# Performance work log

Measured on AMD Instinct MI355X. Metric: run time of the kernel, lower is better.

## Reference

```python
import jax, jax.numpy as jnp
import numpy as np

B, T, D_IN, H, NC = 256, 512, 40, 128, 7


def _lstm_dir(x, W_ih, W_hh, b):
    # x: [B,T,D]; W_ih: [4H,D]; W_hh: [4H,H]; b: [4H] (b_ih+b_hh combined)
    pre = jnp.einsum('btd,gd->btg', x, W_ih) + b  # [B,T,4H]
    h0 = jnp.zeros((x.shape[0], W_hh.shape[1]), x.dtype)
    c0 = jnp.zeros_like(h0)

    def step(carry, p_t):
        h, c = carry
        g = p_t + h @ W_hh.T  # [B,4H]
        i, f, gg, o = jnp.split(g, 4, axis=-1)  # PyTorch gate order: i,f,g,o
        i = jax.nn.sigmoid(i)
        f = jax.nn.sigmoid(f)
        gg = jnp.tanh(gg)
        o = jax.nn.sigmoid(o)
        c = f * c + i * gg
        h = o * jnp.tanh(c)
        return (h, c), h

    _, hs = jax.lax.scan(step, (h0, c0), jnp.swapaxes(pre, 0, 1))  # [T,B,H]
    return jnp.swapaxes(hs, 0, 1)  # [B,T,H]


def _bilstm_layer(x, Wf, Uf, bf, Wr, Ur, br):
    fwd = _lstm_dir(x, Wf, Uf, bf)
    rev = _lstm_dir(x[:, ::-1], Wr, Ur, br)[:, ::-1]
    return jnp.concatenate([fwd, rev], axis=-1)  # [B,T,2H]


def setup_inputs() -> dict:
    key = jax.random.key(0)
    ks = jax.random.split(key, 20)
    s = 1.0 / np.sqrt(H)  # PyTorch LSTM init scale

    def u(k, shape):
        return jax.random.uniform(k, shape, jnp.float32, -s, s)

    inp = {
        'x': jax.random.normal(ks[0], (B, T, D_IN), jnp.float32),
        # layer 0 (input dim 40)
        'W_ih_l0_f': u(ks[1], (4 * H, D_IN)), 'W_hh_l0_f': u(ks[2], (4 * H, H)), 'b_l0_f': u(ks[3], (4 * H,)),
        'W_ih_l0_r': u(ks[4], (4 * H, D_IN)), 'W_hh_l0_r': u(ks[5], (4 * H, H)), 'b_l0_r': u(ks[6], (4 * H,)),
        # layer 1 (input dim 2H)
        'W_ih_l1_f': u(ks[7], (4 * H, 2 * H)), 'W_hh_l1_f': u(ks[8], (4 * H, H)), 'b_l1_f': u(ks[9], (4 * H,)),
        'W_ih_l1_r': u(ks[10], (4 * H, 2 * H)), 'W_hh_l1_r': u(ks[11], (4 * H, H)), 'b_l1_r': u(ks[12], (4 * H,)),
        # classifier head
        'fc_w': u(ks[13], (NC, 2 * H)), 'fc_b': u(ks[14], (NC,)),
    }
    return inp


def reference(x, W_ih_l0_f, W_hh_l0_f, b_l0_f, W_ih_l0_r, W_hh_l0_r, b_l0_r,
              W_ih_l1_f, W_hh_l1_f, b_l1_f, W_ih_l1_r, W_hh_l1_r, b_l1_r,
              fc_w, fc_b):
    h1 = _bilstm_layer(x, W_ih_l0_f, W_hh_l0_f, b_l0_f, W_ih_l0_r, W_hh_l0_r, b_l0_r)
    h2 = _bilstm_layer(h1, W_ih_l1_f, W_hh_l1_f, b_l1_f, W_ih_l1_r, W_hh_l1_r, b_l1_r)
    last = h2[:, -1, :]  # [B,2H]; dropout is identity at eval time
    return last @ fc_w.T + fc_b  # [B,NC]
```

## Files before the change

kernel.cpp:

```cpp
#include <hip/hip_runtime.h>
#include <hip/hip_bf16.h>
#include <type_traits>

typedef short short8 __attribute__((ext_vector_type(8)));
typedef short short4v __attribute__((ext_vector_type(4)));
typedef float f32x4 __attribute__((ext_vector_type(4)));
typedef __bf16 bf16x8 __attribute__((ext_vector_type(8)));

#define DEVI static __device__ __forceinline__

#if __has_builtin(__builtin_amdgcn_exp2f)
#define EXP2(x) __builtin_amdgcn_exp2f(x)
#else
#define EXP2(x) exp2f(x)
#endif
#if __has_builtin(__builtin_amdgcn_rcpf)
#define RCP(x) __builtin_amdgcn_rcpf(x)
#else
#define RCP(x) (1.0f / (x))
#endif

static constexpr int BB = 256, TT = 512, DIN0 = 40, HH = 128, NCLS = 7;
static constexpr float L2E = 1.44269504088896f;

DEVI short f2b(float x) {
  union { __hip_bfloat16 h; short s; } u;
  u.h = __float2bfloat16(x);
  return u.s;
}
DEVI bf16x8 as_bf(short8 s) { return __builtin_bit_cast(bf16x8, s); }
DEVI float b2f(short s) {
  union { unsigned u; float f; } v;
  v.u = ((unsigned)(unsigned short)s) << 16;
  return v.f;
}

DEVI void bar_lgkm() {
  asm volatile("s_waitcnt lgkmcnt(0)\n\ts_barrier" ::: "memory");
}

DEVI f32x4 inv4(f32x4 d) {
  float p1 = d[0] * d[1];
  float p2 = p1 * d[2];
  float p3 = p2 * d[3];
  float R = RCP(p3);
  f32x4 r;
  r[3] = R * p2;
  float R2 = R * d[3];
  r[2] = R2 * p1;
  float R1 = R2 * d[2];
  r[1] = R1 * d[0];
  r[0] = R1 * d[1];
  return r;
}

__global__ __launch_bounds__(512) void rec0(
    const float* __restrict__ x0,
    const float* __restrict__ Wih_f, const float* __restrict__ Whh_f,
    const float* __restrict__ b_f, const float* __restrict__ Wih_r,
    const float* __restrict__ Whh_r, const float* __restrict__ b_r,
    short* __restrict__ h1_out) {
  __shared__ short Hb[2][16][16][8];
  __shared__ short X2[2][8][16][8];

  const int tid = threadIdx.x, w = tid >> 6, lane = tid & 63;
  const int lg = lane >> 4, bcol = lane & 15;
  const int dir = blockIdx.x & 1, b0 = (blockIdx.x >> 1) * 16;
  const int j0 = w * 16 + lg * 4;
  const float* __restrict__ Wih = dir ? Wih_r : Wih_f;
  const float* __restrict__ Whh = dir ? Whh_r : Whh_f;
  const float* __restrict__ bias = dir ? b_r : b_f;
  auto tmap = [&](int s) { return dir ? (TT - 1 - s) : s; };

  short8 wx[4][2], wh[4][4];
  f32x4 bq[4];
#pragma unroll
  for (int q = 0; q < 4; ++q) {
    const float scale = (q == 2) ? (2.0f * L2E) : (-L2E);
    const int m = q * HH + w * 16 + bcol;
#pragma unroll
    for (int kk = 0; kk < 2; ++kk) {
      short8 f;
#pragma unroll
      for (int e = 0; e < 8; ++e) {
        const int k = kk * 32 + lg * 8 + e;
        float v = (k < DIN0) ? Wih[(size_t)m * DIN0 + k] : 0.0f;
        f[e] = f2b(v * scale);
      }
      wx[q][kk] = f;
    }
#pragma unroll
    for (int kk = 0; kk < 4; ++kk) {
      short8 f;
#pragma unroll
      for (int e = 0; e < 8; ++e)
        f[e] = f2b(Whh[(size_t)m * HH + kk * 32 + lg * 8 + e] * scale);
      wh[q][kk] = f;
    }
#pragma unroll
    for (int r = 0; r < 4; ++r) bq[q][r] = bias[q * HH + j0 + r] * scale;
  }

  for (int i = tid; i < 2 * 16 * 16 * 4; i += 512) ((int*)Hb)[i] = 0;
  for (int i = tid; i < 2 * 8 * 16 * 4; i += 512) ((int*)X2)[i] = 0;
  __syncthreads();

  auto load_x = [&](int s) -> f32x4 {
    f32x4 v = {0.f, 0.f, 0.f, 0.f};
    if (tid < 160) {
      int ss = (s < TT) ? s : (TT - 1);
      v = *(const f32x4*)(x0 + ((size_t)(b0 + tid / 10) * TT + tmap(ss)) * DIN0 + (tid % 10) * 4);
    }
    return v;
  };
  auto stage_x = [&](int buf, const f32x4& v) {
    if (tid < 160) {
      short4v o;
      o[0] = f2b(v[0]); o[1] = f2b(v[1]); o[2] = f2b(v[2]); o[3] = f2b(v[3]);
      const int row = tid / 10, c4 = tid % 10;
      *(short4v*)&X2[buf][c4 >> 1][row][(c4 & 1) * 4] = o;
    }
  };
  auto prefill = [&](f32x4* acc, int p) {
#pragma unroll
    for (int kk = 0; kk < 2; ++kk) {
      const bf16x8 bx = as_bf(*(const short8*)&X2[p][kk * 4 + lg][bcol][0]);
#pragma unroll
      for (int q = 0; q < 4; ++q)
        acc[q] = __builtin_amdgcn_mfma_f32_16x16x32_bf16(
            as_bf(wx[q][kk]), bx, (kk == 0) ? bq[q] : acc[q], 0, 0, 0);
    }
  };

  f32x4 cst = {0.f, 0.f, 0.f, 0.f};
  auto cell = [&](f32x4* a, int cur, int s) {
    f32x4 Ei, Ef, Eg, Eo;
#pragma unroll
    for (int r = 0; r < 4; ++r) {
      Ei[r] = EXP2(fminf(a[0][r], 30.f));
      Ef[r] = EXP2(fminf(a[1][r], 30.f));
      Eg[r] = EXP2(fminf(a[2][r], 30.f));
      Eo[r] = EXP2(fminf(a[3][r], 30.f));
    }
    const f32x4 one = {1.f, 1.f, 1.f, 1.f};
    f32x4 si = inv4(one + Ei), sf = inv4(one + Ef);
    f32x4 gd = inv4(one + Eg), so = inv4(one + Eo);
    f32x4 Ec;
#pragma unroll
    for (int r = 0; r < 4; ++r) {
      float tg = 1.f - 2.f * gd[r];
      cst[r] = sf[r] * cst[r] + si[r] * tg;
      Ec[r] = EXP2(fminf(cst[r] * (2.f * L2E), 30.f));
    }
    f32x4 cd = inv4(one + Ec);
    short4v hp;
#pragma unroll
    for (int r = 0; r < 4; ++r) hp[r] = f2b(so[r] * (1.f - 2.f * cd[r]));
    *(short4v*)&Hb[cur ^ 1][j0 >> 3][bcol][j0 & 7] = hp;
    *(short4v*)(h1_out + (((size_t)(b0 + bcol) * TT + tmap(s)) << 8) + dir * HH + j0) = hp;
  };

  stage_x(0, load_x(0));
  stage_x(1, load_x(1));
  f32x4 xst = load_x(2);
  __syncthreads();
  f32x4 accA[4], accB[4];
  prefill(accA, 0);
  bar_lgkm();

  auto stepf = [&](int s, int cur, f32x4* acc, f32x4* accN) {
#pragma unroll
    for (int kk = 0; kk < 4; ++kk) {
      const bf16x8 bh = as_bf(*(const short8*)&Hb[cur][kk * 4 + lg][bcol][0]);
#pragma unroll
      for (int q = 0; q < 4; ++q)
        acc[q] = __builtin_amdgcn_mfma_f32_16x16x32_bf16(as_bf(wh[q][kk]), bh, acc[q], 0, 0, 0);
    }
    cell(acc, cur, s);
    stage_x(cur, xst);
    xst = load_x(s + 3);
    prefill(accN, cur ^ 1);
    bar_lgkm();
  };
  for (int s = 0; s < TT; s += 2) {
    stepf(s, 0, accA, accB);
    stepf(s + 1, 1, accB, accA);
  }
}

template <typename PT>
__global__ __launch_bounds__(512) void pre1(
    const short* __restrict__ h1, const float* __restrict__ Wih_f,
    const float* __restrict__ b_f, const float* __restrict__ Wih_r,
    const float* __restrict__ b_r, PT* __restrict__ pre) {
  __shared__ short X[16 * 256];
  const int tid = threadIdx.x, w = tid >> 6, lane = tid & 63;
  const int lg = lane >> 4, bcol = lane & 15;
  const int gid = blockIdx.x;
  const int dir = gid & 1, tc = (gid >> 1) & 63, bt = gid >> 7;
  const float* __restrict__ Wih = dir ? Wih_r : Wih_f;
  const float* __restrict__ bias = dir ? b_r : b_f;
  const int b0 = bt * 16;

  short8 wx[4][8];
  f32x4 bq[4];
#pragma unroll
  for (int q = 0; q < 4; ++q) {
    const float scale = (q == 2) ? (2.0f * L2E) : (-L2E);
    const int m = q * HH + w * 16 + bcol;
#pragma unroll
    for (int kk = 0; kk < 8; ++kk) {
      short8 f;
#pragma unroll
      for (int e = 0; e < 8; ++e)
        f[e] = f2b(Wih[(size_t)m * 256 + kk * 32 + lg * 8 + e] * scale);
      wx[q][kk] = f;
    }
#pragma unroll
    for (int r = 0; r < 4; ++r) bq[q][r] = bias[q * HH + w * 16 + lg * 4 + r] * scale;
  }

  const int srow = tid >> 5, sch = tid & 31;
  for (int i = 0; i < 8; ++i) {
    const int t = tc * 8 + i;
    short8 v = *(const short8*)(h1 + (((size_t)(b0 + srow) * TT + t) << 8) + sch * 8);
    *(short8*)((char*)X + srow * 512 + ((sch * 16) ^ ((srow & 7) << 4))) = v;
    __syncthreads();
    f32x4 acc[4] = {bq[0], bq[1], bq[2], bq[3]};
#pragma unroll
    for (int kk = 0; kk < 8; ++kk) {
      const bf16x8 bx = as_bf(*(const short8*)((const char*)X + bcol * 512 +
                                               ((kk * 64 + lg * 16) ^ ((bcol & 7) << 4))));
#pragma unroll
      for (int q = 0; q < 4; ++q)
        acc[q] = __builtin_amdgcn_mfma_f32_16x16x32_bf16(as_bf(wx[q][kk]), bx, acc[q], 0, 0, 0);
    }
    PT* op = pre + ((((size_t)dir * 16 + bt) * TT + t) * 8 + w) * 1024 +
             (size_t)(lg * 16 + bcol) * 4;
#pragma unroll
    for (int q = 0; q < 4; ++q) {
      if constexpr (std::is_same_v<PT, float>) {
        *(f32x4*)(op + q * 256) = acc[q];
      } else {
        short4v o;
        o[0] = f2b(acc[q][0]); o[1] = f2b(acc[q][1]);
        o[2] = f2b(acc[q][2]); o[3] = f2b(acc[q][3]);
        *(short4v*)(op + q * 256) = o;
      }
    }
    __syncthreads();
  }
}

template <typename PT>
__global__ __launch_bounds__(512) void rec1(
    const PT* __restrict__ pre, const float* __restrict__ Whh_f,
    const float* __restrict__ Whh_r, float* __restrict__ h2last) {
  __shared__ short Hb[2][16][16][8];
  const int tid = threadIdx.x, w = tid >> 6, lane = tid & 63;
  const int lg = lane >> 4, bcol = lane & 15;
  const int dir = blockIdx.x & 1, bt = blockIdx.x >> 1;
  const int b0 = bt * 16, j0 = w * 16 + lg * 4;
  const float* __restrict__ Whh = dir ? Whh_r : Whh_f;
  auto tmap = [&](int s) { return dir ? (TT - 1 - s) : s; };

  short8 wh[4][4];
#pragma unroll
  for (int q = 0; q < 4; ++q) {
    const float scale = (q == 2) ? (2.0f * L2E) : (-L2E);
    const int m = q * HH + w * 16 + bcol;
#pragma unroll
    for (int kk = 0; kk < 4; ++kk) {
      short8 f;
#pragma unroll
      for (int e = 0; e < 8; ++e)
        f[e] = f2b(Whh[(size_t)m * HH + kk * 32 + lg * 8 + e] * scale);
      wh[q][kk] = f;
    }
  }
  for (int i = tid; i < 2 * 16 * 16 * 4; i += 512) ((int*)Hb)[i] = 0;
  __syncthreads();

  const size_t laneoff = (size_t)(lg * 16 + bcol) * 4;
  auto loadp = [&](f32x4* p, int s) {
    int ss = (s < TT) ? s : (TT - 1);
    const PT* base = pre + ((((size_t)dir * 16 + bt) * TT + tmap(ss)) * 8 + w) * 1024 + laneoff;
#pragma unroll
    for (int q = 0; q < 4; ++q) {
      if constexpr (std::is_same_v<PT, float>) {
        p[q] = *(const f32x4*)(base + q * 256);
      } else {
        short4v v = *(const short4v*)(base + q * 256);
        p[q][0] = b2f(v[0]); p[q][1] = b2f(v[1]);
        p[q][2] = b2f(v[2]); p[q][3] = b2f(v[3]);
      }
    }
  };

  f32x4 cst = {0.f, 0.f, 0.f, 0.f};
  auto stepf = [&](int s, int cur, f32x4* pX) {
    f32x4 acc[4] = {pX[0], pX[1], pX[2], pX[3]};
#pragma unroll
    for (int kk = 0; kk < 4; ++kk) {
      const bf16x8 bh = as_bf(*(const short8*)&Hb[cur][kk * 4 + lg][bcol][0]);
#pragma unroll
      for (int q = 0; q < 4; ++q)
        acc[q] = __builtin_amdgcn_mfma_f32_16x16x32_bf16(as_bf(wh[q][kk]), bh, acc[q], 0, 0, 0);
    }
    f32x4 Ei, Ef, Eg, Eo;
#pragma unroll
    for (int r = 0; r < 4; ++r) {
      Ei[r] = EXP2(fminf(acc[0][r], 30.f));
      Ef[r] = EXP2(fminf(acc[1][r], 30.f));
      Eg[r] = EXP2(fminf(acc[2][r], 30.f));
      Eo[r] = EXP2(fminf(acc[3][r], 30.f));
    }
    const f32x4 one = {1.f, 1.f, 1.f, 1.f};
    f32x4 si = inv4(one + Ei), sf = inv4(one + Ef);
    f32x4 gd = inv4(one + Eg), so = inv4(one + Eo);
    f32x4 Ec;
#pragma unroll
    for (int r = 0; r < 4; ++r) {
      float tg = 1.f - 2.f * gd[r];
      cst[r] = sf[r] * cst[r] + si[r] * tg;
      Ec[r] = EXP2(fminf(cst[r] * (2.f * L2E), 30.f));
    }
    f32x4 cd = inv4(one + Ec);
    short4v hp;
    f32x4 hf;
#pragma unroll
    for (int r = 0; r < 4; ++r) {
      float hv = so[r] * (1.f - 2.f * cd[r]);
      hf[r] = hv;
      hp[r] = f2b(hv);
    }
    *(short4v*)&Hb[cur ^ 1][j0 >> 3][bcol][j0 & 7] = hp;
    if ((dir == 0 && s == TT - 1) || (dir == 1 && s == 0))
      *(f32x4*)(h2last + ((size_t)(b0 + bcol) << 8) + dir * HH + j0) = hf;
    loadp(pX, s + 2);
    bar_lgkm();
  };

  f32x4 pA[4], pB[4];
  loadp(pA, 0);
  loadp(pB, 1);
  for (int s = 0; s < TT; s += 2) {
    stepf(s, 0, pA);
    stepf(s + 1, 1, pB);
  }
}

__global__ __launch_bounds__(512) void rec1_fused(
    const short* __restrict__ h1, const float* __restrict__ Wih_f,
    const float* __restrict__ Whh_f, const float* __restrict__ b_f,
    const float* __restrict__ Wih_r, const float* __restrict__ Whh_r,
    const float* __restrict__ b_r, float* __restrict__ h2last) {
  __shared__ short Hb[2][16][16][8];
  __shared__ char Xraw[16384];

  const int tid = threadIdx.x, w = tid >> 6, lane = tid & 63;
  const int lg = lane >> 4, bcol = lane & 15;
  const int dir = blockIdx.x & 1, b0 = (blockIdx.x >> 1) * 16;
  const int j0 = w * 16 + lg * 4;
  const float* __restrict__ Wih = dir ? Wih_r : Wih_f;
  const float* __restrict__ Whh = dir ? Whh_r : Whh_f;
  const float* __restrict__ bias = dir ? b_r : b_f;
  auto tmap = [&](int s) { return dir ? (TT - 1 - s) : s; };

  short8 wx[4][8], wh[4][4];
  f32x4 bq[4];
#pragma unroll
  for (int q = 0; q < 4; ++q) {
    const float scale = (q == 2) ? (2.0f * L2E) : (-L2E);
    const int m = q * HH + w * 16 + bcol;
#pragma unroll
    for (int kk = 0; kk < 8; ++kk) {
      short8 f;
#pragma unroll
      for (int e = 0; e < 8; ++e)
        f[e] = f2b(Wih[(size_t)m * 256 + kk * 32 + lg * 8 + e] * scale);
      wx[q][kk] = f;
    }
#pragma unroll
    for (int kk = 0; kk < 4; ++kk) {
      short8 f;
#pragma unroll
      for (int e = 0; e < 8; ++e)
        f[e] = f2b(Whh[(size_t)m * HH + kk * 32 + lg * 8 + e] * scale);
      wh[q][kk] = f;
    }
#pragma unroll
    for (int r = 0; r < 4; ++r) bq[q][r] = bias[q * HH + j0 + r] * scale;
  }
  for (int i = tid; i < 2 * 16 * 16 * 4; i += 512) ((int*)Hb)[i] = 0;
  __syncthreads();

  const int xr1 = tid >> 5;
  const int xcb = ((tid << 4) ^ (((tid >> 5) & 7) << 4)) & 511;
  auto ldx = [&](int p, int kk) -> short8 {
    int byte = ((bcol << 9) + (kk << 6) + (lg << 4)) ^ ((bcol & 7) << 4);
    return *(const short8*)(Xraw + p * 8192 + byte);
  };
  auto ldg = [&](int s) -> short8 {
    int ss = (s < TT) ? s : (TT - 1);
    return *(const short8*)((const char*)h1 + (((size_t)(b0 + xr1) * TT + tmap(ss)) << 9) + xcb);
  };

  {
    short8 v0 = ldg(0), v1 = ldg(1);
    *(short8*)(Xraw + tid * 16) = v0;
    *(short8*)(Xraw + 8192 + tid * 16) = v1;
  }
  short8 xstage = ldg(2);
  __syncthreads();

  f32x4 acc[4] = {bq[0], bq[1], bq[2], bq[3]};
#pragma unroll
  for (int kk = 0; kk < 8; ++kk) {
    bf16x8 bx = as_bf(ldx(0, kk));
#pragma unroll
    for (int q = 0; q < 4; ++q)
      acc[q] = __builtin_amdgcn_mfma_f32_16x16x32_bf16(as_bf(wx[q][kk]), bx, acc[q], 0, 0, 0);
  }
  bar_lgkm();

  f32x4 cst = {0.f, 0.f, 0.f, 0.f};
  auto stepf = [&](int s, int buf) {
    *(short8*)(Xraw + buf * 8192 + tid * 16) = xstage;
    xstage = ldg(s + 3);
#pragma unroll
    for (int kk = 0; kk < 4; ++kk) {
      bf16x8 bh = as_bf(*(const short8*)&Hb[buf][kk * 4 + lg][bcol][0]);
#pragma unroll
      for (int q = 0; q < 4; ++q)
        acc[q] = __builtin_amdgcn_mfma_f32_16x16x32_bf16(as_bf(wh[q][kk]), bh, acc[q], 0, 0, 0);
    }
    f32x4 Ei, Ef, Eg, Eo;
#pragma unroll
    for (int r = 0; r < 4; ++r) {
      Ei[r] = EXP2(fminf(acc[0][r], 30.f));
      Ef[r] = EXP2(fminf(acc[1][r], 30.f));
      Eg[r] = EXP2(fminf(acc[2][r], 30.f));
      Eo[r] = EXP2(fminf(acc[3][r], 30.f));
    }
    const f32x4 one = {1.f, 1.f, 1.f, 1.f};
    f32x4 si = inv4(one + Ei), sf = inv4(one + Ef);
    f32x4 gd = inv4(one + Eg), so = inv4(one + Eo);
    f32x4 Ec;
#pragma unroll
    for (int r = 0; r < 4; ++r) {
      float tg = 1.f - 2.f * gd[r];
      cst[r] = sf[r] * cst[r] + si[r] * tg;
      Ec[r] = EXP2(fminf(cst[r] * (2.f * L2E), 30.f));
    }
    f32x4 cd = inv4(one + Ec);
    short4v hp;
    f32x4 hf;
#pragma unroll
    for (int r = 0; r < 4; ++r) {
      float hv = so[r] * (1.f - 2.f * cd[r]);
      hf[r] = hv;
      hp[r] = f2b(hv);
    }
    *(short4v*)&Hb[buf ^ 1][j0 >> 3][bcol][j0 & 7] = hp;
    if ((dir == 0 && s == TT - 1) || (dir == 1 && s == 0))
      *(f32x4*)(h2last + ((size_t)(b0 + bcol) << 8) + dir * HH + j0) = hf;
#pragma unroll
    for (int q = 0; q < 4; ++q) acc[q] = bq[q];
#pragma unroll
    for (int kk = 0; kk < 8; ++kk) {
      bf16x8 bx = as_bf(ldx(buf ^ 1, kk));
#pragma unroll
      for (int q = 0; q < 4; ++q)
        acc[q] = __builtin_amdgcn_mfma_f32_16x16x32_bf16(as_bf(wx[q][kk]), bx, acc[q], 0, 0, 0);
    }
    bar_lgkm();
  };
  for (int s = 0; s < TT; s += 2) {
    stepf(s, 0);
    stepf(s + 1, 1);
  }
}

__global__ void fc_kernel(const float* __restrict__ h2last,
                          const float* __restrict__ fcw,
                          const float* __restrict__ fcb,
                          float* __restrict__ out) {
  const int gid = blockIdx.x * blockDim.x + threadIdx.x;
  if (gid >= BB * NCLS) return;
  const int b = gid / NCLS, n = gid % NCLS;
  const float* hp = h2last + (size_t)b * 256;
  const float* wp = fcw + (size_t)n * 256;
  float s = fcb[n];
#pragma unroll 8
  for (int j = 0; j < 256; ++j) s = fmaf(hp[j], wp[j], s);
  out[gid] = s;
}

extern "C" void kernel_launch(void* const* d_in, const int* in_sizes, int n_in,
                              void* d_out, int out_size, void* d_ws, size_t ws_size,
                              hipStream_t stream) {
  const float* x     = (const float*)d_in[0];
  const float* Wih0f = (const float*)d_in[1];
  const float* Whh0f = (const float*)d_in[2];
  const float* b0f   = (const float*)d_in[3];
  const float* Wih0r = (const float*)d_in[4];
  const float* Whh0r = (const float*)d_in[5];
  const float* b0r   = (const float*)d_in[6];
  const float* Wih1f = (const float*)d_in[7];
  const float* Whh1f = (const float*)d_in[8];
  const float* b1f   = (const float*)d_in[9];
  const float* Wih1r = (const float*)d_in[10];
  const float* Whh1r = (const float*)d_in[11];
  const float* b1r   = (const float*)d_in[12];
  const float* fcw   = (const float*)d_in[13];
  const float* fcb   = (const float*)d_in[14];

  short* h1 = (short*)d_ws;
  float* h2last = (float*)((char*)d_ws + (64ull << 20));
  char* prebuf = (char*)d_ws + (64ull << 20) + (1ull << 20);

  const size_t preElems = 2ull * 16 * TT * 8 * 1024;
  const size_t baseBytes = (64ull << 20) + (1ull << 20);

  rec0<<<dim3(32), dim3(512), 0, stream>>>(
      x, Wih0f, Whh0f, b0f, Wih0r, Whh0r, b0r, h1);

  if (ws_size >= baseBytes + preElems * 4) {
    float* pre = (float*)prebuf;
    pre1<float><<<dim3(2048), dim3(512), 0, stream>>>(h1, Wih1f, b1f, Wih1r, b1r, pre);
    rec1<float><<<dim3(32), dim3(512), 0, stream>>>(pre, Whh1f, Whh1r, h2last);
  } else if (ws_size >= baseBytes + preElems * 2) {
    short* pre = (short*)prebuf;
    pre1<short><<<dim3(2048), dim3(512), 0, stream>>>(h1, Wih1f, b1f, Wih1r, b1r, pre);
    rec1<short><<<dim3(32), dim3(512), 0, stream>>>(pre, Whh1f, Whh1r, h2last);
  } else {
    rec1_fused<<<dim3(32), dim3(512), 0, stream>>>(
        h1, Wih1f, Whh1f, b1f, Wih1r, Whh1r, b1r, h2last);
  }

  fc_kernel<<<dim3((BB * NCLS + 255) / 256), dim3(256), 0, stream>>>(
      h2last, fcw, fcb, (float*)d_out);
}
```

Before: 1.230 ms.

## Replace precomputed-input layer-1 path with fused recurrent kernel using split accumulators

```diff
diff --git a/kernel.cpp b/kernel.cpp
--- a/kernel.cpp
+++ b/kernel.cpp
@@ -1,6 +1,5 @@
 #include <hip/hip_runtime.h>
 #include <hip/hip_bf16.h>
-#include <type_traits>
 
 typedef short short8 __attribute__((ext_vector_type(8)));
 typedef short short4v __attribute__((ext_vector_type(4)));
@@ -29,11 +28,6 @@
   return u.s;
 }
 DEVI bf16x8 as_bf(short8 s) { return __builtin_bit_cast(bf16x8, s); }
-DEVI float b2f(short s) {
-  union { unsigned u; float f; } v;
-  v.u = ((unsigned)(unsigned short)s) << 16;
-  return v.f;
-}
 
 DEVI void bar_lgkm() {
   asm volatile("s_waitcnt lgkmcnt(0)\n\ts_barrier" ::: "memory");
@@ -188,175 +182,14 @@
   }
 }
 
-template <typename PT>
-__global__ __launch_bounds__(512) void pre1(
-    const short* __restrict__ h1, const float* __restrict__ Wih_f,
-    const float* __restrict__ b_f, const float* __restrict__ Wih_r,
-    const float* __restrict__ b_r, PT* __restrict__ pre) {
-  __shared__ short X[16 * 256];
-  const int tid = threadIdx.x, w = tid >> 6, lane = tid & 63;
-  const int lg = lane >> 4, bcol = lane & 15;
-  const int gid = blockIdx.x;
-  const int dir = gid & 1, tc = (gid >> 1) & 63, bt = gid >> 7;
-  const float* __restrict__ Wih = dir ? Wih_r : Wih_f;
-  const float* __restrict__ bias = dir ? b_r : b_f;
-  const int b0 = bt * 16;
-
-  short8 wx[4][8];
-  f32x4 bq[4];
-#pragma unroll
-  for (int q = 0; q < 4; ++q) {
-    const float scale = (q == 2) ? (2.0f * L2E) : (-L2E);
-    const int m = q * HH + w * 16 + bcol;
-#pragma unroll
-    for (int kk = 0; kk < 8; ++kk) {
-      short8 f;
-#pragma unroll
-      for (int e = 0; e < 8; ++e)
-        f[e] = f2b(Wih[(size_t)m * 256 + kk * 32 + lg * 8 + e] * scale);
-      wx[q][kk] = f;
-    }
-#pragma unroll
-    for (int r = 0; r < 4; ++r) bq[q][r] = bias[q * HH + w * 16 + lg * 4 + r] * scale;
-  }
-
-  const int srow = tid >> 5, sch = tid & 31;
-  for (int i = 0; i < 8; ++i) {
-    const int t = tc * 8 + i;
-    short8 v = *(const short8*)(h1 + (((size_t)(b0 + srow) * TT + t) << 8) + sch * 8);
-    *(short8*)((char*)X + srow * 512 + ((sch * 16) ^ ((srow & 7) << 4))) = v;
-    __syncthreads();
-    f32x4 acc[4] = {bq[0], bq[1], bq[2], bq[3]};
-#pragma unroll
-    for (int kk = 0; kk < 8; ++kk) {
-      const bf16x8 bx = as_bf(*(const short8*)((const char*)X + bcol * 512 +
-                                               ((kk * 64 + lg * 16) ^ ((bcol & 7) << 4))));
-#pragma unroll
-      for (int q = 0; q < 4; ++q)
-        acc[q] = __builtin_amdgcn_mfma_f32_16x16x32_bf16(as_bf(wx[q][kk]), bx, acc[q], 0, 0, 0);
-    }
-    PT* op = pre + ((((size_t)dir * 16 + bt) * TT + t) * 8 + w) * 1024 +
-             (size_t)(lg * 16 + bcol) * 4;
-#pragma unroll
-    for (int q = 0; q < 4; ++q) {
-      if constexpr (std::is_same_v<PT, float>) {
-        *(f32x4*)(op + q * 256) = acc[q];
-      } else {
-        short4v o;
-        o[0] = f2b(acc[q][0]); o[1] = f2b(acc[q][1]);
-        o[2] = f2b(acc[q][2]); o[3] = f2b(acc[q][3]);
-        *(short4v*)(op + q * 256) = o;
-      }
-    }
-    __syncthreads();
-  }
-}
-
-template <typename PT>
-__global__ __launch_bounds__(512) void rec1(
-    const PT* __restrict__ pre, const float* __restrict__ Whh_f,
-    const float* __restrict__ Whh_r, float* __restrict__ h2last) {
-  __shared__ short Hb[2][16][16][8];
-  const int tid = threadIdx.x, w = tid >> 6, lane = tid & 63;
-  const int lg = lane >> 4, bcol = lane & 15;
-  const int dir = blockIdx.x & 1, bt = blockIdx.x >> 1;
-  const int b0 = bt * 16, j0 = w * 16 + lg * 4;
-  const float* __restrict__ Whh = dir ? Whh_r : Whh_f;
-  auto tmap = [&](int s) { return dir ? (TT - 1 - s) : s; };
-
-  short8 wh[4][4];
-#pragma unroll
-  for (int q = 0; q < 4; ++q) {
-    const float scale = (q == 2) ? (2.0f * L2E) : (-L2E);
-    const int m = q * HH + w * 16 + bcol;
-#pragma unroll
-    for (int kk = 0; kk < 4; ++kk) {
-      short8 f;
-#pragma unroll
-      for (int e = 0; e < 8; ++e)
-        f[e] = f2b(Whh[(size_t)m * HH + kk * 32 + lg * 8 + e] * scale);
-      wh[q][kk] = f;
-    }
-  }
-  for (int i = tid; i < 2 * 16 * 16 * 4; i += 512) ((int*)Hb)[i] = 0;
-  __syncthreads();
-
-  const size_t laneoff = (size_t)(lg * 16 + bcol) * 4;
-  auto loadp = [&](f32x4* p, int s) {
-    int ss = (s < TT) ? s : (TT - 1);
-    const PT* base = pre + ((((size_t)dir * 16 + bt) * TT + tmap(ss)) * 8 + w) * 1024 + laneoff;
-#pragma unroll
-    for (int q = 0; q < 4; ++q) {
-      if constexpr (std::is_same_v<PT, float>) {
-        p[q] = *(const f32x4*)(base + q * 256);
-      } else {
-        short4v v = *(const short4v*)(base + q * 256);
-        p[q][0] = b2f(v[0]); p[q][1] = b2f(v[1]);
-        p[q][2] = b2f(v[2]); p[q][3] = b2f(v[3]);
-      }
-    }
-  };
-
-  f32x4 cst = {0.f, 0.f, 0.f, 0.f};
-  auto stepf = [&](int s, int cur, f32x4* pX) {
-    f32x4 acc[4] = {pX[0], pX[1], pX[2], pX[3]};
-#pragma unroll
-    for (int kk = 0; kk < 4; ++kk) {
-      const bf16x8 bh = as_bf(*(const short8*)&Hb[cur][kk * 4 + lg][bcol][0]);
-#pragma unroll
-      for (int q = 0; q < 4; ++q)
-        acc[q] = __builtin_amdgcn_mfma_f32_16x16x32_bf16(as_bf(wh[q][kk]), bh, acc[q], 0, 0, 0);
-    }
-    f32x4 Ei, Ef, Eg, Eo;
-#pragma unroll
-    for (int r = 0; r < 4; ++r) {
-      Ei[r] = EXP2(fminf(acc[0][r], 30.f));
-      Ef[r] = EXP2(fminf(acc[1][r], 30.f));
-      Eg[r] = EXP2(fminf(acc[2][r], 30.f));
-      Eo[r] = EXP2(fminf(acc[3][r], 30.f));
-    }
-    const f32x4 one = {1.f, 1.f, 1.f, 1.f};
-    f32x4 si = inv4(one + Ei), sf = inv4(one + Ef);
-    f32x4 gd = inv4(one + Eg), so = inv4(one + Eo);
-    f32x4 Ec;
-#pragma unroll
-    for (int r = 0; r < 4; ++r) {
-      float tg = 1.f - 2.f * gd[r];
-      cst[r] = sf[r] * cst[r] + si[r] * tg;
-      Ec[r] = EXP2(fminf(cst[r] * (2.f * L2E), 30.f));
-    }
-    f32x4 cd = inv4(one + Ec);
-    short4v hp;
-    f32x4 hf;
-#pragma unroll
-    for (int r = 0; r < 4; ++r) {
-      float hv = so[r] * (1.f - 2.f * cd[r]);
-      hf[r] = hv;
-      hp[r] = f2b(hv);
-    }
-    *(short4v*)&Hb[cur ^ 1][j0 >> 3][bcol][j0 & 7] = hp;
-    if ((dir == 0 && s == TT - 1) || (dir == 1 && s == 0))
-      *(f32x4*)(h2last + ((size_t)(b0 + bcol) << 8) + dir * HH + j0) = hf;
-    loadp(pX, s + 2);
-    bar_lgkm();
-  };
-
-  f32x4 pA[4], pB[4];
-  loadp(pA, 0);
-  loadp(pB, 1);
-  for (int s = 0; s < TT; s += 2) {
-    stepf(s, 0, pA);
-    stepf(s + 1, 1, pB);
-  }
-}
-
-__global__ __launch_bounds__(512) void rec1_fused(
+__global__ __launch_bounds__(512, 2) void rec1v2(
     const short* __restrict__ h1, const float* __restrict__ Wih_f,
     const float* __restrict__ Whh_f, const float* __restrict__ b_f,
     const float* __restrict__ Wih_r, const float* __restrict__ Whh_r,
     const float* __restrict__ b_r, float* __restrict__ h2last) {
   __shared__ short Hb[2][16][16][8];
-  __shared__ char Xraw[16384];
+  __shared__ char Xs[2][16384];
+  __shared__ float bqs[8][4][4][4];
 
   const int tid = threadIdx.x, w = tid >> 6, lane = tid & 63;
   const int lg = lane >> 4, bcol = lane & 15;
@@ -368,7 +201,6 @@
   auto tmap = [&](int s) { return dir ? (TT - 1 - s) : s; };
 
   short8 wx[4][8], wh[4][4];
-  f32x4 bq[4];
 #pragma unroll
   for (int q = 0; q < 4; ++q) {
     const float scale = (q == 2) ? (2.0f * L2E) : (-L2E);
@@ -389,52 +221,76 @@
         f[e] = f2b(Whh[(size_t)m * HH + kk * 32 + lg * 8 + e] * scale);
       wh[q][kk] = f;
     }
-#pragma unroll
-    for (int r = 0; r < 4; ++r) bq[q][r] = bias[q * HH + j0 + r] * scale;
+  }
+  {
+    const int bw = tid >> 6, blgq = tid & 63;
+    const int blg = blgq >> 4, bqq = (blgq >> 2) & 3, brr = blgq & 3;
+    const float scale = (bqq == 2) ? (2.0f * L2E) : (-L2E);
+    bqs[bw][blg][bqq][brr] = bias[bqq * HH + bw * 16 + blg * 4 + brr] * scale;
   }
   for (int i = tid; i < 2 * 16 * 16 * 4; i += 512) ((int*)Hb)[i] = 0;
   __syncthreads();
 
-  const int xr1 = tid >> 5;
-  const int xcb = ((tid << 4) ^ (((tid >> 5) & 7) << 4)) & 511;
-  auto ldx = [&](int p, int kk) -> short8 {
-    int byte = ((bcol << 9) + (kk << 6) + (lg << 4)) ^ ((bcol & 7) << 4);
-    return *(const short8*)(Xraw + p * 8192 + byte);
-  };
+  const int srow = tid >> 5, sseg = tid & 31;
+  const int swz_w = ((sseg * 16 + srow) << 4) ^ ((sseg & 7) << 4);
   auto ldg = [&](int s) -> short8 {
     int ss = (s < TT) ? s : (TT - 1);
-    return *(const short8*)((const char*)h1 + (((size_t)(b0 + xr1) * TT + tmap(ss)) << 9) + xcb);
-  };
-
-  {
-    short8 v0 = ldg(0), v1 = ldg(1);
-    *(short8*)(Xraw + tid * 16) = v0;
-    *(short8*)(Xraw + 8192 + tid * 16) = v1;
-  }
+    return *(const short8*)(h1 + (((size_t)(b0 + srow) * TT + tmap(ss)) << 8) + sseg * 8);
+  };
+  auto stage_x = [&](int buf, const short8& v) {
+    *(short8*)(Xs[buf] + swz_w) = v;
+  };
+  auto ldx = [&](int p, int kk) -> short8 {
+    const int koct = kk * 4 + lg;
+    const int byte = (((koct * 16 + bcol) << 4)) ^ ((koct & 7) << 4);
+    return *(const short8*)(Xs[p] + byte);
+  };
+
+  f32x4 acc[4], acc2[4];
+  auto prefill = [&](int p) {
+#pragma unroll
+    for (int q = 0; q < 4; ++q) {
+      acc[q] = *(const f32x4*)&bqs[w][lg][q][0];
+      acc2[q] = f32x4{0.f, 0.f, 0.f, 0.f};
+    }
+#pragma unroll
+    for (int kk = 0; kk < 4; ++kk) {
+      const bf16x8 bx = as_bf(ldx(p, kk));
+      const bf16x8 bx2 = as_bf(ldx(p, kk + 4));
+#pragma unroll
+      for (int q = 0; q < 4; ++q) {
+        acc[q] = __builtin_amdgcn_mfma_f32_16x16x32_bf16(as_bf(wx[q][kk]), bx, acc[q], 0, 0, 0);
+        acc2[q] = __builtin_amdgcn_mfma_f32_16x16x32_bf16(as_bf(wx[q][kk + 4]), bx2, acc2[q], 0, 0, 0);
+      }
+    }
+  };
+
+  stage_x(0, ldg(0));
+  stage_x(1, ldg(1));
   short8 xstage = ldg(2);
   __syncthreads();
-
-  f32x4 acc[4] = {bq[0], bq[1], bq[2], bq[3]};
-#pragma unroll
-  for (int kk = 0; kk < 8; ++kk) {
-    bf16x8 bx = as_bf(ldx(0, kk));
-#pragma unroll
-    for (int q = 0; q < 4; ++q)
-      acc[q] = __builtin_amdgcn_mfma_f32_16x16x32_bf16(as_bf(wx[q][kk]), bx, acc[q], 0, 0, 0);
-  }
+  prefill(0);
   bar_lgkm();
 
   f32x4 cst = {0.f, 0.f, 0.f, 0.f};
-  auto stepf = [&](int s, int buf) {
-    *(short8*)(Xraw + buf * 8192 + tid * 16) = xstage;
+
+  auto stepf = [&](int s, int cur) {
+    stage_x(cur, xstage);
     xstage = ldg(s + 3);
-#pragma unroll
-    for (int kk = 0; kk < 4; ++kk) {
-      bf16x8 bh = as_bf(*(const short8*)&Hb[buf][kk * 4 + lg][bcol][0]);
-#pragma unroll
-      for (int q = 0; q < 4; ++q)
+
+#pragma unroll
+    for (int kk = 0; kk < 2; ++kk) {
+      const bf16x8 bh = as_bf(*(const short8*)&Hb[cur][kk * 4 + lg][bcol][0]);
+      const bf16x8 bh2 = as_bf(*(const short8*)&Hb[cur][(kk + 2) * 4 + lg][bcol][0]);
+#pragma unroll
+      for (int q = 0; q < 4; ++q) {
         acc[q] = __builtin_amdgcn_mfma_f32_16x16x32_bf16(as_bf(wh[q][kk]), bh, acc[q], 0, 0, 0);
-    }
+        acc2[q] = __builtin_amdgcn_mfma_f32_16x16x32_bf16(as_bf(wh[q][kk + 2]), bh2, acc2[q], 0, 0, 0);
+      }
+    }
+#pragma unroll
+    for (int q = 0; q < 4; ++q) acc[q] += acc2[q];
+
     f32x4 Ei, Ef, Eg, Eo;
 #pragma unroll
     for (int r = 0; r < 4; ++r) {
@@ -462,20 +318,14 @@
       hf[r] = hv;
       hp[r] = f2b(hv);
     }
-    *(short4v*)&Hb[buf ^ 1][j0 >> 3][bcol][j0 & 7] = hp;
+    *(short4v*)&Hb[cur ^ 1][j0 >> 3][bcol][j0 & 7] = hp;
     if ((dir == 0 && s == TT - 1) || (dir == 1 && s == 0))
       *(f32x4*)(h2last + ((size_t)(b0 + bcol) << 8) + dir * HH + j0) = hf;
-#pragma unroll
-    for (int q = 0; q < 4; ++q) acc[q] = bq[q];
-#pragma unroll
-    for (int kk = 0; kk < 8; ++kk) {
-      bf16x8 bx = as_bf(ldx(buf ^ 1, kk));
-#pragma unroll
-      for (int q = 0; q < 4; ++q)
-        acc[q] = __builtin_amdgcn_mfma_f32_16x16x32_bf16(as_bf(wx[q][kk]), bx, acc[q], 0, 0, 0);
-    }
+
+    prefill(cur ^ 1);
     bar_lgkm();
   };
+
   for (int s = 0; s < TT; s += 2) {
     stepf(s, 0);
     stepf(s + 1, 1);
@@ -518,27 +368,11 @@
 
   short* h1 = (short*)d_ws;
   float* h2last = (float*)((char*)d_ws + (64ull << 20));
-  char* prebuf = (char*)d_ws + (64ull << 20) + (1ull << 20);
-
-  const size_t preElems = 2ull * 16 * TT * 8 * 1024;
-  const size_t baseBytes = (64ull << 20) + (1ull << 20);
 
   rec0<<<dim3(32), dim3(512), 0, stream>>>(
       x, Wih0f, Whh0f, b0f, Wih0r, Whh0r, b0r, h1);
-
-  if (ws_size >= baseBytes + preElems * 4) {
-    float* pre = (float*)prebuf;
-    pre1<float><<<dim3(2048), dim3(512), 0, stream>>>(h1, Wih1f, b1f, Wih1r, b1r, pre);
-    rec1<float><<<dim3(32), dim3(512), 0, stream>>>(pre, Whh1f, Whh1r, h2last);
-  } else if (ws_size >= baseBytes + preElems * 2) {
-    short* pre = (short*)prebuf;
-    pre1<short><<<dim3(2048), dim3(512), 0, stream>>>(h1, Wih1f, b1f, Wih1r, b1r, pre);
-    rec1<short><<<dim3(32), dim3(512), 0, stream>>>(pre, Whh1f, Whh1r, h2last);
-  } else {
-    rec1_fused<<<dim3(32), dim3(512), 0, stream>>>(
-        h1, Wih1f, Whh1f, b1f, Wih1r, Whh1r, b1r, h2last);
-  }
-
+  rec1v2<<<dim3(32), dim3(512), 0, stream>>>(
+      h1, Wih1f, Whh1f, b1f, Wih1r, Whh1r, b1r, h2last);
   fc_kernel<<<dim3((BB * NCLS + 255) / 256), dim3(256), 0, stream>>>(
       h2last, fcw, fcb, (float*)d_out);
 }
```

Result: slower. 1.406 ms (+14.3%).
